# Optimization experiments

Hardware: AMD Instinct MI355X
Metric: run time of the kernel (lower is better)

Reference implementation:

```python
import jax, jax.numpy as jnp
import numpy as np

B, S, H, NH, DH, DFF = 4, 8192, 2048, 16, 128, 8192
K = 1024
EPS = 1e-5
THETA = 10000.0
SCALE_FACTOR = 1.0
SCALE_GAP = 1.0


def setup_inputs() -> dict:
    key = jax.random.key(0)
    ks = jax.random.split(key, 12)
    hidden_states = jax.random.normal(ks[0], (B, S, H), dtype=jnp.float32)
    position_ids = jnp.broadcast_to(jnp.arange(S, dtype=jnp.int32)[None, :], (B, S))
    # exactly K routed tokens per row -> static compacted length (matches torch
    # path when all rows have equal top-k counts)
    rowkeys = jax.random.split(ks[1], B)
    sel = jax.vmap(lambda k: jax.random.permutation(k, S)[:K])(rowkeys)  # [B,K]
    topk_mask = jnp.zeros((B, S), dtype=bool).at[jnp.arange(B)[:, None], sel].set(True)
    topk_scores = jax.random.uniform(ks[2], (B,), dtype=jnp.float32)
    w = lambda k, shp: (jax.random.normal(k, shp, dtype=jnp.float32) * 0.02)
    return {
        "hidden_states": hidden_states,
        "position_ids": position_ids,
        "topk_mask": topk_mask,
        "topk_scores": topk_scores,
        "topk_k": K,
        "Wq": w(ks[3], (H, H)),
        "Wk": w(ks[4], (H, H)),
        "Wv": w(ks[5], (H, H)),
        "Wo": w(ks[6], (H, H)),
        "Wgate": w(ks[7], (H, DFF)),
        "Wup": w(ks[8], (H, DFF)),
        "Wdown": w(ks[9], (DFF, H)),
        "ln1_w": jnp.ones((H,), dtype=jnp.float32),
        "ln2_w": jnp.ones((H,), dtype=jnp.float32),
    }


def _rmsnorm(x, w):
    return x * jax.lax.rsqrt(jnp.mean(x * x, axis=-1, keepdims=True) + EPS) * w


def _rotate_half(x):
    x1, x2 = jnp.split(x, 2, axis=-1)
    return jnp.concatenate([-x2, x1], axis=-1)


def reference(hidden_states, position_ids, topk_mask, topk_scores, topk_k,
              Wq, Wk, Wv, Wo, Wgate, Wup, Wdown, ln1_w, ln2_w):
    Kk = int(topk_k)
    b, s, h = hidden_states.shape
    # true positions first, in original order (stable) -> compacted indices
    order = jnp.argsort(jnp.where(topk_mask, 0, 1).astype(jnp.int32), axis=1, stable=True)
    topk_idx = order[:, :Kk]                              # [B,K]
    bidx = jnp.arange(b)[:, None]
    # 🔍 dispatch: gather routed tokens into compact [B,K,H]
    x = hidden_states[bidx, topk_idx]
    pos = position_ids[bidx, topk_idx]                    # original positions for RoPE

    residual = x
    hs = _rmsnorm(x, ln1_w)
    q = (hs @ Wq).reshape(b, Kk, NH, DH).transpose(0, 2, 1, 3)
    k = (hs @ Wk).reshape(b, Kk, NH, DH).transpose(0, 2, 1, 3)
    v = (hs @ Wv).reshape(b, Kk, NH, DH).transpose(0, 2, 1, 3)
    inv_freq = 1.0 / (THETA ** (jnp.arange(0, DH, 2, dtype=jnp.float32) / DH))
    freqs = pos[..., None].astype(jnp.float32) * inv_freq  # [B,K,DH/2]
    emb = jnp.concatenate([freqs, freqs], axis=-1)
    cos = jnp.cos(emb)[:, None, :, :]
    sin = jnp.sin(emb)[:, None, :, :]
    q = q * cos + _rotate_half(q) * sin
    k = k * cos + _rotate_half(k) * sin
    scores = jnp.einsum('bhqd,bhkd->bhqk', q, k) / np.sqrt(DH).astype(np.float32)
    causal = jnp.tril(jnp.ones((Kk, Kk), dtype=bool))
    scores = jnp.where(causal, scores, jnp.finfo(scores.dtype).min)
    attn = jax.nn.softmax(scores, axis=-1)
    o = jnp.einsum('bhqk,bhkd->bhqd', attn, v).transpose(0, 2, 1, 3).reshape(b, Kk, H)
    hs = residual + o @ Wo

    residual2 = hs
    m = _rmsnorm(hs, ln2_w)
    m = (jax.nn.silu(m @ Wgate) * (m @ Wup)) @ Wdown

    # rescale_hidden_states=True path
    scale = 0.5 * SCALE_FACTOR + (topk_scores - 0.5) * SCALE_GAP  # [B]
    out_gathered = residual2 + m * scale[:, None, None]
    # 🔍 combine: scatter routed outputs back; bottom tokens pass through unchanged
    out = hidden_states.at[bidx, topk_idx].set(out_gathered)
    return out
```

## Files before the change

### kernel.cpp

```cpp
#include <hip/hip_runtime.h>
#include <hip/hip_bf16.h>
#include <stdint.h>

#define Bb 4
#define Ss 8192
#define Hh 2048
#define NHh 16
#define DHh 128
#define DFFf 8192
#define KS 1024
#define NTOK 4096

typedef unsigned short u16;
typedef __bf16 bf16x8 __attribute__((ext_vector_type(8)));
typedef float f32x4 __attribute__((ext_vector_type(4)));

union B8 { uint4 u; bf16x8 v; u16 s[8]; };

__device__ __forceinline__ float b2f(u16 x) { return __uint_as_float(((unsigned)x) << 16); }
__device__ __forceinline__ u16 f2b(float x) {
  __hip_bfloat16 h = __float2bfloat16(x);
  return *reinterpret_cast<u16*>(&h);
}

__device__ __forceinline__ void gll16(const void* g, void* l) {
  __builtin_amdgcn_global_load_lds((const __attribute__((address_space(1))) void*)g,
                                   (__attribute__((address_space(3))) void*)l, 16, 0, 0);
}

__device__ __forceinline__ int swz16(int r, int cg) {
  int u = ((r & 1) << 2) | cg;
  return ((r >> 1) << 3) | (u ^ ((r >> 1) & 7));
}

__global__ void topk_prep(const void* maskp, const int* __restrict__ posids,
                          const float* __restrict__ scores,
                          int* __restrict__ idx, int* __restrict__ posg,
                          float* __restrict__ scalev) {
  int b = blockIdx.x;
  int tid = threadIdx.x, lane = tid & 63, wv = tid >> 6;
  __shared__ int wsum[4];
  __shared__ int base;
  __shared__ int mode;
  __shared__ int detCnt;
  if (tid == 0) { base = 0; detCnt = 0; }
  __syncthreads();
  {
    const unsigned char* mb = (const unsigned char*)maskp;
    int c = 0;
    for (int s = tid; s < 8192; s += 256) c += (mb[s] != 0);
    atomicAdd(&detCnt, c);
  }
  __syncthreads();
  if (tid == 0) mode = (detCnt == KS) ? 1 : 0;
  __syncthreads();
  const unsigned char* mb = (const unsigned char*)maskp;
  const int* mi = (const int*)maskp;
  for (int s0 = 0; s0 < Ss; s0 += 256) {
    int s = s0 + tid;
    int pred = mode ? (mb[(size_t)b * Ss + s] != 0) : (mi[(size_t)b * Ss + s] != 0);
    unsigned long long bal = __ballot(pred);
    int lp = __popcll(bal & ((1ull << lane) - 1ull));
    int wtot = __popcll(bal);
    if (lane == 0) wsum[wv] = wtot;
    __syncthreads();
    int woff = 0;
    for (int w = 0; w < wv; ++w) woff += wsum[w];
    int tot = wsum[0] + wsum[1] + wsum[2] + wsum[3];
    int p = base + woff + lp;
    if (pred && p < KS) {
      idx[b * KS + p] = s;
      posg[b * KS + p] = posids[(size_t)b * Ss + s];
    }
    __syncthreads();
    if (tid == 0) base += tot;
    __syncthreads();
  }
  if (b == 0 && tid < Bb) scalev[tid] = 0.5f * 1.0f + (scores[tid] - 0.5f) * 1.0f;
}

template <int MODE>
__global__ void transpose_w(const float* __restrict__ in, u16* __restrict__ out, int R, int C) {
  __shared__ float tile[32][33];
  int tx = threadIdx.x, ty = threadIdx.y;
  int c0 = blockIdx.x * 32, r0 = blockIdx.y * 32;
  for (int j = ty; j < 32; j += 8) tile[j][tx] = in[(size_t)(r0 + j) * C + c0 + tx];
  __syncthreads();
  for (int j = ty; j < 32; j += 8) {
    int c = c0 + j;
    size_t row = (MODE == 0) ? c : (size_t)((c >> 5) << 6) + (c & 31) + (MODE == 2 ? 32 : 0);
    out[row * R + r0 + tx] = f2b(tile[tx][j]);
  }
}

template <int GATHER>
__global__ __launch_bounds__(256) void rmsnorm_k(const float* __restrict__ src0,
                                                 const int* __restrict__ idx,
                                                 const float* __restrict__ w,
                                                 u16* __restrict__ out) {
  int t = blockIdx.x;
  const float* src;
  if (GATHER) { int b = t >> 10; src = src0 + ((size_t)b * Ss + idx[t]) * Hh; }
  else src = src0 + (size_t)t * Hh;
  int tid = threadIdx.x, lane = tid & 63, wv = tid >> 6;
  float4 x0 = *(const float4*)(src + tid * 8);
  float4 x1 = *(const float4*)(src + tid * 8 + 4);
  float ss = x0.x * x0.x + x0.y * x0.y + x0.z * x0.z + x0.w * x0.w +
             x1.x * x1.x + x1.y * x1.y + x1.z * x1.z + x1.w * x1.w;
  for (int o = 32; o; o >>= 1) ss += __shfl_down(ss, o);
  __shared__ float wred[4];
  if (lane == 0) wred[wv] = ss;
  __syncthreads();
  float tot = wred[0] + wred[1] + wred[2] + wred[3];
  float r = rsqrtf(tot * (1.0f / Hh) + 1e-5f);
  const float* wp = w + tid * 8;
  u16* op = out + (size_t)t * Hh + tid * 8;
  float xs[8] = {x0.x, x0.y, x0.z, x0.w, x1.x, x1.y, x1.z, x1.w};
#pragma unroll
  for (int j = 0; j < 8; ++j) op[j] = f2b(xs[j] * r * wp[j]);
}

template <int EPI>
__global__ __launch_bounds__(512, 2) void gemm256(
    const u16* __restrict__ A, const u16* __restrict__ Bt,
    int N, int Kd, int lda, int gm, int gw,
    u16* __restrict__ Cb,
    const float* __restrict__ hid, const int* __restrict__ idx,
    const float* __restrict__ hs2, const float* __restrict__ scalev,
    float* __restrict__ Cf) {
  __shared__ u16 lds[65536];
  int bid = blockIdx.x;
  int xcd = bid & 7;
  int i2 = bid >> 3;
  int bm = i2 / gw;
  int bn = xcd * gw + i2 % gw;
  int m0 = bm * 256, n0 = bn * 256;
  int tid = threadIdx.x, lane = tid & 63, wv = tid >> 6;
  int wm = wv >> 2, wn = wv & 3;
  int NT = Kd >> 6;

  int P16 = wv * 64 + lane;
  int blk = P16 >> 3, up = P16 & 7;
  int uu = up ^ (blk & 7);
  int r0 = blk * 2 + (uu >> 2), cg0 = uu & 3;
  const u16* srcA = A + (size_t)(m0 + r0) * lda + cg0 * 8;
  const u16* srcB = Bt + (size_t)(n0 + r0) * Kd + cg0 * 8;
  size_t rsA = (size_t)128 * lda, rsB = (size_t)128 * Kd;

  int offA = swz16(wm * 128 + (lane & 15), lane >> 4) * 8;
  int offB = 32768 + swz16(wn * 64 + (lane & 15), lane >> 4) * 8;
  u16* ldsw = &lds[wv * 512];

  f32x4 acc[8][4] = {};
  B8 aR[4], bR[4];

  gll16(srcB,      ldsw + 32768); gll16(srcB + rsB,      ldsw + 36864);
  gll16(srcA,      ldsw +     0); gll16(srcA + rsA,      ldsw +  4096);
  gll16(srcB + 32, ldsw + 40960); gll16(srcB + 32 + rsB, ldsw + 45056);
  gll16(srcA + 32, ldsw +  8192); gll16(srcA + 32 + rsA, ldsw + 12288);
  gll16(srcB + 64, ldsw + 49152); gll16(srcB + 64 + rsB, ldsw + 53248);
  gll16(srcA + 64, ldsw + 16384); gll16(srcA + 64 + rsA, ldsw + 20480);
  gll16(srcB + 96, ldsw + 57344); gll16(srcB + 96 + rsB, ldsw + 61440);
  asm volatile("s_waitcnt vmcnt(6)" ::: "memory");
  asm volatile("s_barrier" ::: "memory");

  const u16* stA = srcA + 64;
  const u16* stB = srcB + 64;

  auto phase = [&](int abase, int bbase, int mh) {
    if (mh == 0) {
#pragma unroll
      for (int nf = 0; nf < 4; ++nf) bR[nf].u = *(const uint4*)&lds[offB + bbase + nf * 512];
    }
#pragma unroll
    for (int i3 = 0; i3 < 4; ++i3)
      aR[i3].u = *(const uint4*)&lds[offA + abase + (i3 + 4 * mh) * 512];
  };
  auto mfma16 = [&](int mh) {
    asm volatile("s_barrier" ::: "memory");
    asm volatile("s_waitcnt lgkmcnt(0)" ::: "memory");
    __builtin_amdgcn_s_setprio(1);
#pragma unroll
    for (int nf = 0; nf < 4; ++nf)
#pragma unroll
      for (int i3 = 0; i3 < 4; ++i3)
        acc[mh * 4 + i3][nf] =
            __builtin_amdgcn_mfma_f32_16x16x32_bf16(aR[i3].v, bR[nf].v, acc[mh * 4 + i3][nf], 0, 0, 0);
    __builtin_amdgcn_s_setprio(0);
  };

  for (int ktp = 0; ktp < NT; ktp += 2) {
    bool sAll = (ktp < NT - 2);
    phase(0, 0, 0);
    { gll16(stA + 32, ldsw + 24576); gll16(stA + 32 + rsA, ldsw + 28672); }
    mfma16(0);
    asm volatile("s_barrier" ::: "memory");
    phase(0, 0, 1);
    if (sAll) { gll16(stB + 64, ldsw + 32768); gll16(stB + 64 + rsB, ldsw + 36864); }
    mfma16(1);
    asm volatile("s_barrier" ::: "memory");
    phase(8192, 8192, 0);
    if (sAll) { gll16(stA + 64, ldsw + 0); gll16(stA + 64 + rsA, ldsw + 4096); }
    mfma16(0);
    asm volatile("s_barrier" ::: "memory");
    phase(8192, 8192, 1);
    if (sAll) { gll16(stB + 96, ldsw + 40960); gll16(stB + 96 + rsB, ldsw + 45056); }
    mfma16(1);
    if (sAll) asm volatile("s_waitcnt vmcnt(6)" ::: "memory");
    else asm volatile("s_waitcnt vmcnt(0)" ::: "memory");
    asm volatile("s_barrier" ::: "memory");
    phase(16384, 16384, 0);
    if (sAll) { gll16(stA + 96, ldsw + 8192); gll16(stA + 96 + rsA, ldsw + 12288); }
    mfma16(0);
    asm volatile("s_barrier" ::: "memory");
    phase(16384, 16384, 1);
    if (sAll) { gll16(stB + 128, ldsw + 49152); gll16(stB + 128 + rsB, ldsw + 53248); }
    mfma16(1);
    asm volatile("s_barrier" ::: "memory");
    phase(24576, 24576, 0);
    if (sAll) { gll16(stA + 128, ldsw + 16384); gll16(stA + 128 + rsA, ldsw + 20480); }
    mfma16(0);
    asm volatile("s_barrier" ::: "memory");
    phase(24576, 24576, 1);
    if (sAll) { gll16(stB + 160, ldsw + 57344); gll16(stB + 160 + rsB, ldsw + 61440); }
    mfma16(1);
    if (sAll) asm volatile("s_waitcnt vmcnt(6)" ::: "memory");
    asm volatile("s_barrier" ::: "memory");
    stA += 128; stB += 128;
  }

  if (EPI == 4) {
    int gcol0 = ((n0 + wn * 64) >> 1) + (lane & 15);
#pragma unroll
    for (int mf = 0; mf < 8; ++mf) {
#pragma unroll
      for (int rr = 0; rr < 4; ++rr) {
        int row = m0 + wm * 128 + mf * 16 + (lane >> 4) * 4 + rr;
#pragma unroll
        for (int nf = 0; nf < 2; ++nf) {
          float g = acc[mf][nf][rr];
          float u = acc[mf][nf + 2][rr];
          Cb[(size_t)row * 8192 + gcol0 + nf * 16] = f2b(g / (1.0f + __expf(-g)) * u);
        }
      }
    }
    return;
  }

#pragma unroll
  for (int mf = 0; mf < 8; ++mf) {
#pragma unroll
    for (int rr = 0; rr < 4; ++rr) {
      int row = m0 + wm * 128 + mf * 16 + (lane >> 4) * 4 + rr;
#pragma unroll
      for (int nf = 0; nf < 4; ++nf) {
        int col = n0 + wn * 64 + nf * 16 + (lane & 15);
        float v = acc[mf][nf][rr];
        if (EPI == 0) {
          Cb[(size_t)row * N + col] = f2b(v);
        } else if (EPI == 1) {
          int b = row >> 10;
          Cf[(size_t)row * Hh + col] = hid[((size_t)b * Ss + idx[row]) * Hh + col] + v;
        } else {
          int b = row >> 10;
          Cf[((size_t)b * Ss + idx[row]) * Hh + col] = hs2[(size_t)row * Hh + col] + v * scalev[b];
        }
      }
    }
  }
}

template <int EPI>
__global__ __launch_bounds__(512, 2) void gemm128(
    const u16* __restrict__ A, const u16* __restrict__ Bt,
    int N, int Kd, int lda, int gm, int gw,
    u16* __restrict__ Cb,
    const float* __restrict__ hid, const int* __restrict__ idx,
    const float* __restrict__ hs2, const float* __restrict__ scalev,
    float* __restrict__ Cf, u16* __restrict__ vTout) {
  __shared__ u16 lds[49152];
  int bid = blockIdx.x;
  int xcd = bid & 7;
  int i2 = bid >> 3;
  int bm = i2 / gw;
  int bn = xcd * gw + i2 % gw;
  int m0 = bm * 128, n0 = bn * 256;
  int tid = threadIdx.x, lane = tid & 63, wv = tid >> 6;
  int wm = wv >> 2, wn = wv & 3;
  int NT = Kd >> 6;

  int P16 = wv * 64 + lane;
  int blk = P16 >> 3, up = P16 & 7;
  int uu = up ^ (blk & 7);
  int r0 = blk * 2 + (uu >> 2), cg0 = uu & 3;
  const u16* srcA = A + (size_t)(m0 + r0) * lda + cg0 * 8;
  const u16* srcB = Bt + (size_t)(n0 + r0) * Kd + cg0 * 8;
  size_t rsB = (size_t)128 * Kd;

  int offB = swz16(wn * 64 + (lane & 15), lane >> 4) * 8;
  int offA = 32768 + swz16(wm * 64 + (lane & 15), lane >> 4) * 8;
  u16* ldsw = &lds[wv * 512];

  f32x4 acc[4][4] = {};
  B8 aR[4], bR[4];

  gll16(srcB,      ldsw +     0); gll16(srcB + rsB,      ldsw +  4096); gll16(srcA,      ldsw + 32768);
  gll16(srcB + 32, ldsw +  8192); gll16(srcB + 32 + rsB, ldsw + 12288); gll16(srcA + 32, ldsw + 36864);
  gll16(srcB + 64, ldsw + 16384); gll16(srcB + 64 + rsB, ldsw + 20480); gll16(srcA + 64, ldsw + 40960);
  asm volatile("s_waitcnt vmcnt(6)" ::: "memory");
  asm volatile("s_barrier" ::: "memory");

  const u16* stA = srcA + 64;
  const u16* stB = srcB + 64;

  auto rd = [&](int s) {
#pragma unroll
    for (int f = 0; f < 4; ++f) bR[f].u = *(const uint4*)&lds[offB + s * 8192 + f * 512];
#pragma unroll
    for (int f = 0; f < 4; ++f) aR[f].u = *(const uint4*)&lds[offA + s * 4096 + f * 512];
  };
  auto mfma16 = [&]() {
    asm volatile("s_barrier" ::: "memory");
    asm volatile("s_waitcnt lgkmcnt(0)" ::: "memory");
    __builtin_amdgcn_s_setprio(1);
#pragma unroll
    for (int nf = 0; nf < 4; ++nf)
#pragma unroll
      for (int mf = 0; mf < 4; ++mf)
        acc[mf][nf] = __builtin_amdgcn_mfma_f32_16x16x32_bf16(aR[mf].v, bR[nf].v, acc[mf][nf], 0, 0, 0);
    __builtin_amdgcn_s_setprio(0);
  };

  for (int ktp = 0; ktp < NT; ktp += 2) {
    bool sAll = (ktp < NT - 2);
    rd(0);
    { gll16(stB + 32, ldsw + 24576); gll16(stB + 32 + rsB, ldsw + 28672); gll16(stA + 32, ldsw + 45056); }
    mfma16();
    asm volatile("s_waitcnt vmcnt(6)" ::: "memory");
    asm volatile("s_barrier" ::: "memory");
    rd(1);
    if (sAll) { gll16(stB + 64, ldsw + 0); gll16(stB + 64 + rsB, ldsw + 4096); gll16(stA + 64, ldsw + 32768); }
    mfma16();
    if (sAll) asm volatile("s_waitcnt vmcnt(6)" ::: "memory");
    else asm volatile("s_waitcnt vmcnt(3)" ::: "memory");
    asm volatile("s_barrier" ::: "memory");
    rd(2);
    if (sAll) { gll16(stB + 96, ldsw + 8192); gll16(stB + 96 + rsB, ldsw + 12288); gll16(stA + 96, ldsw + 36864); }
    mfma16();
    if (sAll) asm volatile("s_waitcnt vmcnt(6)" ::: "memory");
    else asm volatile("s_waitcnt vmcnt(0)" ::: "memory");
    asm volatile("s_barrier" ::: "memory");
    rd(3);
    if (sAll) { gll16(stB + 128, ldsw + 16384); gll16(stB + 128 + rsB, ldsw + 20480); gll16(stA + 128, ldsw + 40960); }
    mfma16();
    if (sAll) asm volatile("s_waitcnt vmcnt(6)" ::: "memory");
    asm volatile("s_barrier" ::: "memory");
    stA += 128; stB += 128;
  }

  if (EPI == 3) {
#pragma unroll
    for (int mf = 0; mf < 4; ++mf) {
      int rowb = m0 + wm * 64 + mf * 16 + (lane >> 4) * 4;
      int bb = rowb >> 10, kk2 = rowb & 1023;
#pragma unroll
      for (int nf = 0; nf < 4; ++nf) {
        int col = n0 + wn * 64 + nf * 16 + (lane & 15);
        if (col >= 4096) {
          int hh = (col - 4096) >> 7, dd = (col - 4096) & 127;
          ushort4 pk;
          pk.x = f2b(acc[mf][nf][0]); pk.y = f2b(acc[mf][nf][1]);
          pk.z = f2b(acc[mf][nf][2]); pk.w = f2b(acc[mf][nf][3]);
          *(ushort4*)&vTout[(((size_t)bb * 16 + hh) * 128 + dd) * 1024 + kk2] = pk;
        } else {
#pragma unroll
          for (int rr = 0; rr < 4; ++rr)
            Cb[(size_t)(rowb + rr) * N + col] = f2b(acc[mf][nf][rr]);
        }
      }
    }
    return;
  }

#pragma unroll
  for (int mf = 0; mf < 4; ++mf) {
#pragma unroll
    for (int rr = 0; rr < 4; ++rr) {
      int row = m0 + wm * 64 + mf * 16 + (lane >> 4) * 4 + rr;
#pragma unroll
      for (int nf = 0; nf < 4; ++nf) {
        int col = n0 + wn * 64 + nf * 16 + (lane & 15);
        float v = acc[mf][nf][rr];
        if (EPI == 0) {
          Cb[(size_t)row * N + col] = f2b(v);
        } else if (EPI == 1) {
          int b = row >> 10;
          Cf[(size_t)row * Hh + col] = hid[((size_t)b * Ss + idx[row]) * Hh + col] + v;
        } else {
          int b = row >> 10;
          Cf[((size_t)b * Ss + idx[row]) * Hh + col] = hs2[(size_t)row * Hh + col] + v * scalev[b];
        }
      }
    }
  }
}

__global__ __launch_bounds__(256) void rope_qk(u16* __restrict__ qkv,
                                               const int* __restrict__ posg) {
  int gid = blockIdx.x * 256 + threadIdx.x;
  int i = gid & 63;
  int h = (gid >> 6) & 15;
  int t = gid >> 10;
  float p = (float)posg[t];
  float inv = exp2f(-(float)i * (13.287712379549449f / 64.0f));
  float ang = p * inv;
  float sv, cv;
  __sincosf(ang, &sv, &cv);
  size_t base = (size_t)t * 6144 + h * DHh + i;
  u16* Q = qkv;
  u16* Kq = qkv + 2048;
  float q1 = b2f(Q[base]), q2 = b2f(Q[base + 64]);
  Q[base] = f2b(q1 * cv - q2 * sv);
  Q[base + 64] = f2b(q2 * cv + q1 * sv);
  float k1 = b2f(Kq[base]), k2 = b2f(Kq[base + 64]);
  Kq[base] = f2b(k1 * cv - k2 * sv);
  Kq[base + 64] = f2b(k2 * cv + k1 * sv);
}

__global__ __launch_bounds__(256) void attn_k(const u16* __restrict__ QKV,
                                              const u16* __restrict__ vT,
                                              u16* __restrict__ O) {
  int qb = blockIdx.x;
  int head = blockIdx.y;
  int b = head >> 4, h = head & 15;
  int tid = threadIdx.x, lane = tid & 63, wv = tid >> 6;
  int l15 = lane & 15, lq = lane >> 4, l7 = lane & 7;
  __shared__ __align__(16) u16 KsA[16384];
  __shared__ __align__(16) u16 VtA[16384];
  u16* PsB = &KsA[wv * 2176];

  int keyr = tid >> 4;
  int uphys = tid & 15;
  size_t koff0 = (size_t)keyr * 6144 + ((uphys ^ (keyr & 7)) * 8);
  size_t voff0 = (size_t)keyr * 1024 + ((uphys ^ (keyr & 7)) * 8);
  char* dK = (char*)KsA + wv * 1024;
  char* dV = (char*)VtA + wv * 1024;

  int q0 = qb * 64 + wv * 16;
  int tokQ = b * KS + q0;
  B8 qf[4];
  const u16* qp = QKV + (size_t)(tokQ + l15) * 6144 + h * DHh;
#pragma unroll
  for (int c = 0; c < 4; ++c) qf[c].u = *(const uint4*)(qp + c * 32 + lq * 8);
  float m_run = -1e30f, l_run = 0.0f;
  f32x4 oacc[8] = {};
  int qi = q0 + l15;

  int nt = (qb >> 1) + 1;
  for (int t = 0; t < nt; ++t) {
    int ks = t * 128;
    bool maskTile = (t == nt - 1);
    __syncthreads();
    const u16* kp = QKV + (size_t)(b * KS + ks) * 6144 + 2048 + h * DHh + koff0;
    const u16* vp = vT + ((size_t)head * 128) * 1024 + ks + voff0;
#pragma unroll
    for (int i = 0; i < 8; ++i) {
      gll16(kp + (size_t)i * 16 * 6144, dK + i * 4096);
      gll16(vp + (size_t)i * 16 * 1024, dV + i * 4096);
    }
    asm volatile("s_waitcnt vmcnt(0)" ::: "memory");
    __syncthreads();
    f32x4 st[8] = {};
#pragma unroll
    for (int c = 0; c < 4; ++c) {
#pragma unroll
      for (int kt = 0; kt < 8; ++kt) {
        B8 kf;
        kf.u = *(const uint4*)&KsA[(kt * 16 + l15) * 128 + (((c * 4 + lq) ^ l7) * 8)];
        st[kt] = __builtin_amdgcn_mfma_f32_16x16x32_bf16(kf.v, qf[c].v, st[kt], 0, 0, 0);
      }
    }
    __syncthreads();
    float pmax = -INFINITY;
    if (maskTile) {
#pragma unroll
      for (int kt = 0; kt < 8; ++kt)
#pragma unroll
        for (int r = 0; r < 4; ++r) {
          int ki = ks + kt * 16 + lq * 4 + r;
          float v = st[kt][r] * 0.088388347648318447f;
          v = (ki <= qi) ? v : -INFINITY;
          st[kt][r] = v;
          pmax = fmaxf(pmax, v);
        }
    } else {
#pragma unroll
      for (int kt = 0; kt < 8; ++kt)
#pragma unroll
        for (int r = 0; r < 4; ++r) {
          float v = st[kt][r] * 0.088388347648318447f;
          st[kt][r] = v;
          pmax = fmaxf(pmax, v);
        }
    }
    pmax = fmaxf(pmax, __shfl_xor(pmax, 16));
    pmax = fmaxf(pmax, __shfl_xor(pmax, 32));
    float m_new = fmaxf(m_run, pmax);
    float alpha = __expf(m_run - m_new);
    float psum = 0.0f;
#pragma unroll
    for (int kt = 0; kt < 8; ++kt)
#pragma unroll
      for (int r = 0; r < 4; ++r) {
        float pv = __expf(st[kt][r] - m_new);
        st[kt][r] = pv;
        psum += pv;
      }
    psum += __shfl_xor(psum, 16);
    psum += __shfl_xor(psum, 32);
    l_run = l_run * alpha + psum;
    m_run = m_new;
#pragma unroll
    for (int kt = 0; kt < 8; ++kt) {
      ushort4 pk;
      pk.x = f2b(st[kt][0]); pk.y = f2b(st[kt][1]);
      pk.z = f2b(st[kt][2]); pk.w = f2b(st[kt][3]);
      *(ushort4*)&PsB[l15 * 136 + kt * 16 + lq * 4] = pk;
    }
    B8 pf[4];
#pragma unroll
    for (int kslot = 0; kslot < 4; ++kslot)
      pf[kslot].u = *(const uint4*)&PsB[l15 * 136 + kslot * 32 + lq * 8];
    float al0 = __shfl(alpha, lq * 4 + 0);
    float al1 = __shfl(alpha, lq * 4 + 1);
    float al2 = __shfl(alpha, lq * 4 + 2);
    float al3 = __shfl(alpha, lq * 4 + 3);
#pragma unroll
    for (int dt = 0; dt < 8; ++dt) {
      oacc[dt][0] *= al0; oacc[dt][1] *= al1;
      oacc[dt][2] *= al2; oacc[dt][3] *= al3;
    }
#pragma unroll
    for (int dt = 0; dt < 8; ++dt) {
      int d = dt * 16 + l15;
#pragma unroll
      for (int kslot = 0; kslot < 4; ++kslot) {
        B8 vf;
        vf.u = *(const uint4*)&VtA[d * 128 + (((kslot * 4 + lq) ^ l7) * 8)];
        oacc[dt] = __builtin_amdgcn_mfma_f32_16x16x32_bf16(pf[kslot].v, vf.v, oacc[dt], 0, 0, 0);
      }
    }
  }
  float linv = 1.0f / l_run;
  float li[4];
#pragma unroll
  for (int r = 0; r < 4; ++r) li[r] = __shfl(linv, lq * 4 + r);
#pragma unroll
  for (int r = 0; r < 4; ++r) {
    int tok = tokQ + lq * 4 + r;
    u16* op = O + (size_t)tok * Hh + h * DHh;
#pragma unroll
    for (int dt = 0; dt < 8; ++dt) op[dt * 16 + l15] = f2b(oacc[dt][r] * li[r]);
  }
}

extern "C" void kernel_launch(void* const* d_in, const int* in_sizes, int n_in,
                              void* d_out, int out_size, void* d_ws, size_t ws_size,
                              hipStream_t stream) {
  (void)in_sizes; (void)n_in; (void)out_size; (void)ws_size;
  const float* hid = (const float*)d_in[0];
  const int* posids = (const int*)d_in[1];
  const void* mask = d_in[2];
  const float* scores = (const float*)d_in[3];
  const float* Wq = (const float*)d_in[5];
  const float* Wk = (const float*)d_in[6];
  const float* Wv = (const float*)d_in[7];
  const float* Wo = (const float*)d_in[8];
  const float* Wg = (const float*)d_in[9];
  const float* Wu = (const float*)d_in[10];
  const float* Wd = (const float*)d_in[11];
  const float* ln1 = (const float*)d_in[12];
  const float* ln2 = (const float*)d_in[13];
  float* out = (float*)d_out;
  char* ws = (char*)d_ws;

  u16* WqkvT = (u16*)(ws + 0);
  u16* WoT   = (u16*)(ws + 25165824);
  u16* WguT  = (u16*)(ws + 33554432);
  u16* WdT   = (u16*)(ws + 100663296);
  int* idx   = (int*)(ws + 134217728);
  int* posg  = (int*)(ws + 134217728 + 16384);
  float* scalev = (float*)(ws + 134217728 + 32768);
  char* R = ws + 134283264;
  u16* hsn    = (u16*)(R);
  u16* qkv    = (u16*)(R + 16777216);
  u16* attn_o = (u16*)(R + 67108864);
  u16* vT     = (u16*)(R + 88080384);
  u16* gu2    = (u16*)(R);
  float* hs2  = (float*)(ws + 268500992);
  u16* mnorm  = (u16*)(ws + 302055424);

  hipMemcpyAsync(out, hid, (size_t)Bb * Ss * Hh * 4, hipMemcpyDeviceToDevice, stream);

  topk_prep<<<Bb, 256, 0, stream>>>(mask, posids, scores, idx, posg, scalev);

  transpose_w<0><<<dim3(64, 64), dim3(32, 8), 0, stream>>>(Wq, WqkvT, 2048, 2048);
  transpose_w<0><<<dim3(64, 64), dim3(32, 8), 0, stream>>>(Wk, WqkvT + 2048 * 2048, 2048, 2048);
  transpose_w<0><<<dim3(64, 64), dim3(32, 8), 0, stream>>>(Wv, WqkvT + 4096 * 2048, 2048, 2048);
  transpose_w<0><<<dim3(64, 64), dim3(32, 8), 0, stream>>>(Wo, WoT, 2048, 2048);
  transpose_w<1><<<dim3(256, 64), dim3(32, 8), 0, stream>>>(Wg, WguT, 2048, 8192);
  transpose_w<2><<<dim3(256, 64), dim3(32, 8), 0, stream>>>(Wu, WguT, 2048, 8192);
  transpose_w<0><<<dim3(64, 256), dim3(32, 8), 0, stream>>>(Wd, WdT, 8192, 2048);

  rmsnorm_k<1><<<NTOK, 256, 0, stream>>>(hid, idx, ln1, hsn);

  gemm128<3><<<768, 512, 0, stream>>>(hsn, WqkvT, 6144, 2048, 2048, 32, 3, qkv,
                                      nullptr, nullptr, nullptr, nullptr, nullptr, vT);

  rope_qk<<<16384, 256, 0, stream>>>(qkv, posg);

  attn_k<<<dim3(16, 64), 256, 0, stream>>>(qkv, vT, attn_o);

  gemm128<1><<<256, 512, 0, stream>>>(attn_o, WoT, 2048, 2048, 2048, 32, 1, nullptr,
                                      hid, idx, nullptr, nullptr, hs2, nullptr);

  rmsnorm_k<0><<<NTOK, 256, 0, stream>>>(hs2, nullptr, ln2, mnorm);

  gemm256<4><<<1024, 512, 0, stream>>>(mnorm, WguT, 16384, 2048, 2048, 16, 8, gu2,
                                       nullptr, nullptr, nullptr, nullptr, nullptr);

  gemm128<2><<<256, 512, 0, stream>>>(gu2, WdT, 2048, 8192, 8192, 32, 1, nullptr,
                                      nullptr, idx, hs2, scalev, out, nullptr);
}
```

Before: 1.076 ms.

## Retune gemm128 pipeline, keep P in registers in attention, split gate/up GEMM

```diff
diff --git a/kernel.cpp b/kernel.cpp
--- a/kernel.cpp
+++ b/kernel.cpp
@@ -123,7 +123,7 @@
 template <int EPI>
 __global__ __launch_bounds__(512, 2) void gemm256(
     const u16* __restrict__ A, const u16* __restrict__ Bt,
-    int N, int Kd, int lda, int gm, int gw,
+    int N, int Kd, int lda, int gm, int gw, int nb,
     u16* __restrict__ Cb,
     const float* __restrict__ hid, const int* __restrict__ idx,
     const float* __restrict__ hs2, const float* __restrict__ scalev,
@@ -133,7 +133,7 @@
   int xcd = bid & 7;
   int i2 = bid >> 3;
   int bm = i2 / gw;
-  int bn = xcd * gw + i2 % gw;
+  int bn = xcd * gw + i2 % gw + nb;
   int m0 = bm * 256, n0 = bn * 256;
   int tid = threadIdx.x, lane = tid & 63, wv = tid >> 6;
   int wm = wv >> 2, wn = wv & 3;
@@ -271,14 +271,14 @@
 }
 
 template <int EPI>
-__global__ __launch_bounds__(512, 2) void gemm128(
+__global__ __launch_bounds__(512, 4) void gemm128(
     const u16* __restrict__ A, const u16* __restrict__ Bt,
     int N, int Kd, int lda, int gm, int gw,
     u16* __restrict__ Cb,
     const float* __restrict__ hid, const int* __restrict__ idx,
     const float* __restrict__ hs2, const float* __restrict__ scalev,
     float* __restrict__ Cf, u16* __restrict__ vTout) {
-  __shared__ u16 lds[49152];
+  __shared__ u16 lds[36864];
   int bid = blockIdx.x;
   int xcd = bid & 7;
   int i2 = bid >> 3;
@@ -288,6 +288,7 @@
   int tid = threadIdx.x, lane = tid & 63, wv = tid >> 6;
   int wm = wv >> 2, wn = wv & 3;
   int NT = Kd >> 6;
+  int P = NT * 2;
 
   int P16 = wv * 64 + lane;
   int blk = P16 >> 3, up = P16 & 7;
@@ -298,28 +299,32 @@
   size_t rsB = (size_t)128 * Kd;
 
   int offB = swz16(wn * 64 + (lane & 15), lane >> 4) * 8;
-  int offA = 32768 + swz16(wm * 64 + (lane & 15), lane >> 4) * 8;
+  int offA = swz16(wm * 64 + (lane & 15), lane >> 4) * 8;
   u16* ldsw = &lds[wv * 512];
 
   f32x4 acc[4][4] = {};
   B8 aR[4], bR[4];
 
-  gll16(srcB,      ldsw +     0); gll16(srcB + rsB,      ldsw +  4096); gll16(srcA,      ldsw + 32768);
-  gll16(srcB + 32, ldsw +  8192); gll16(srcB + 32 + rsB, ldsw + 12288); gll16(srcA + 32, ldsw + 36864);
-  gll16(srcB + 64, ldsw + 16384); gll16(srcB + 64 + rsB, ldsw + 20480); gll16(srcA + 64, ldsw + 40960);
-  asm volatile("s_waitcnt vmcnt(6)" ::: "memory");
+  auto stage = [&](int q, int bB, int aB) {
+    const u16* spB = srcB + q * 32;
+    gll16(spB, ldsw + bB);
+    gll16(spB + rsB, ldsw + bB + 4096);
+    gll16(srcA + q * 32, ldsw + aB);
+  };
+
+  stage(0, 0, 24576);
+  stage(1, 8192, 28672);
+  asm volatile("s_waitcnt vmcnt(3)" ::: "memory");
   asm volatile("s_barrier" ::: "memory");
 
-  const u16* stA = srcA + 64;
-  const u16* stB = srcB + 64;
-
-  auto rd = [&](int s) {
-#pragma unroll
-    for (int f = 0; f < 4; ++f) bR[f].u = *(const uint4*)&lds[offB + s * 8192 + f * 512];
-#pragma unroll
-    for (int f = 0; f < 4; ++f) aR[f].u = *(const uint4*)&lds[offA + s * 4096 + f * 512];
-  };
-  auto mfma16 = [&]() {
+  int rB = 0, rA = 24576;
+  int tB = 16384, tA = 32768;
+  for (int p = 0; p < P; ++p) {
+#pragma unroll
+    for (int f = 0; f < 4; ++f) bR[f].u = *(const uint4*)&lds[rB + offB + f * 512];
+#pragma unroll
+    for (int f = 0; f < 4; ++f) aR[f].u = *(const uint4*)&lds[rA + offA + f * 512];
+    if (p + 2 < P) stage(p + 2, tB, tA);
     asm volatile("s_barrier" ::: "memory");
     asm volatile("s_waitcnt lgkmcnt(0)" ::: "memory");
     __builtin_amdgcn_s_setprio(1);
@@ -329,33 +334,12 @@
       for (int mf = 0; mf < 4; ++mf)
         acc[mf][nf] = __builtin_amdgcn_mfma_f32_16x16x32_bf16(aR[mf].v, bR[nf].v, acc[mf][nf], 0, 0, 0);
     __builtin_amdgcn_s_setprio(0);
-  };
-
-  for (int ktp = 0; ktp < NT; ktp += 2) {
-    bool sAll = (ktp < NT - 2);
-    rd(0);
-    { gll16(stB + 32, ldsw + 24576); gll16(stB + 32 + rsB, ldsw + 28672); gll16(stA + 32, ldsw + 45056); }
-    mfma16();
-    asm volatile("s_waitcnt vmcnt(6)" ::: "memory");
-    asm volatile("s_barrier" ::: "memory");
-    rd(1);
-    if (sAll) { gll16(stB + 64, ldsw + 0); gll16(stB + 64 + rsB, ldsw + 4096); gll16(stA + 64, ldsw + 32768); }
-    mfma16();
-    if (sAll) asm volatile("s_waitcnt vmcnt(6)" ::: "memory");
-    else asm volatile("s_waitcnt vmcnt(3)" ::: "memory");
-    asm volatile("s_barrier" ::: "memory");
-    rd(2);
-    if (sAll) { gll16(stB + 96, ldsw + 8192); gll16(stB + 96 + rsB, ldsw + 12288); gll16(stA + 96, ldsw + 36864); }
-    mfma16();
-    if (sAll) asm volatile("s_waitcnt vmcnt(6)" ::: "memory");
-    else asm volatile("s_waitcnt vmcnt(0)" ::: "memory");
-    asm volatile("s_barrier" ::: "memory");
-    rd(3);
-    if (sAll) { gll16(stB + 128, ldsw + 16384); gll16(stB + 128 + rsB, ldsw + 20480); gll16(stA + 128, ldsw + 40960); }
-    mfma16();
-    if (sAll) asm volatile("s_waitcnt vmcnt(6)" ::: "memory");
-    asm volatile("s_barrier" ::: "memory");
-    stA += 128; stB += 128;
+    if (p < P - 2) asm volatile("s_waitcnt vmcnt(3)" ::: "memory");
+    else if (p == P - 2) asm volatile("s_waitcnt vmcnt(0)" ::: "memory");
+    asm volatile("s_barrier" ::: "memory");
+    tB = rB; tA = rA;
+    rB = (rB == 16384) ? 0 : rB + 8192;
+    rA = (rA == 32768) ? 24576 : rA + 4096;
   }
 
   if (EPI == 3) {
@@ -363,6 +347,8 @@
     for (int mf = 0; mf < 4; ++mf) {
       int rowb = m0 + wm * 64 + mf * 16 + (lane >> 4) * 4;
       int bb = rowb >> 10, kk2 = rowb & 1023;
+      int w = kk2 & 127;
+      int kk2p = (kk2 & ~127) | (((((w >> 5) & 3) << 2) + ((w >> 2) & 3)) << 3) | (((w >> 4) & 1) << 2);
 #pragma unroll
       for (int nf = 0; nf < 4; ++nf) {
         int col = n0 + wn * 64 + nf * 16 + (lane & 15);
@@ -371,7 +357,7 @@
           ushort4 pk;
           pk.x = f2b(acc[mf][nf][0]); pk.y = f2b(acc[mf][nf][1]);
           pk.z = f2b(acc[mf][nf][2]); pk.w = f2b(acc[mf][nf][3]);
-          *(ushort4*)&vTout[(((size_t)bb * 16 + hh) * 128 + dd) * 1024 + kk2] = pk;
+          *(ushort4*)&vTout[(((size_t)bb * 16 + hh) * 128 + dd) * 1024 + kk2p] = pk;
         } else {
 #pragma unroll
           for (int rr = 0; rr < 4; ++rr)
@@ -437,12 +423,11 @@
   int l15 = lane & 15, lq = lane >> 4, l7 = lane & 7;
   __shared__ __align__(16) u16 KsA[16384];
   __shared__ __align__(16) u16 VtA[16384];
-  u16* PsB = &KsA[wv * 2176];
-
-  int keyr = tid >> 4;
-  int uphys = tid & 15;
-  size_t koff0 = (size_t)keyr * 6144 + ((uphys ^ (keyr & 7)) * 8);
-  size_t voff0 = (size_t)keyr * 1024 + ((uphys ^ (keyr & 7)) * 8);
+
+  int rr0 = tid >> 4;
+  int u0 = tid & 15;
+  size_t koff0 = (size_t)rr0 * 6144 + ((u0 ^ (rr0 & 7)) * 8);
+  size_t voff0 = (size_t)rr0 * 1024 + ((u0 ^ (rr0 & 7)) * 8);
   char* dK = (char*)KsA + wv * 1024;
   char* dV = (char*)VtA + wv * 1024;
 
@@ -462,13 +447,12 @@
     bool maskTile = (t == nt - 1);
     __syncthreads();
     const u16* kp = QKV + (size_t)(b * KS + ks) * 6144 + 2048 + h * DHh + koff0;
-    const u16* vp = vT + ((size_t)head * 128) * 1024 + ks + voff0;
-#pragma unroll
-    for (int i = 0; i < 8; ++i) {
-      gll16(kp + (size_t)i * 16 * 6144, dK + i * 4096);
-      gll16(vp + (size_t)i * 16 * 1024, dV + i * 4096);
-    }
-    asm volatile("s_waitcnt vmcnt(0)" ::: "memory");
+    const u16* vp = vT + (size_t)head * 131072 + ks + voff0;
+#pragma unroll
+    for (int i = 0; i < 8; ++i) gll16(kp + (size_t)i * 98304, dK + i * 4096);
+#pragma unroll
+    for (int i = 0; i < 8; ++i) gll16(vp + i * 16384, dV + i * 4096);
+    asm volatile("s_waitcnt vmcnt(8)" ::: "memory");
     __syncthreads();
     f32x4 st[8] = {};
 #pragma unroll
@@ -480,7 +464,6 @@
         st[kt] = __builtin_amdgcn_mfma_f32_16x16x32_bf16(kf.v, qf[c].v, st[kt], 0, 0, 0);
       }
     }
-    __syncthreads();
     float pmax = -INFINITY;
     if (maskTile) {
 #pragma unroll
@@ -520,17 +503,16 @@
     psum += __shfl_xor(psum, 32);
     l_run = l_run * alpha + psum;
     m_run = m_new;
-#pragma unroll
-    for (int kt = 0; kt < 8; ++kt) {
-      ushort4 pk;
-      pk.x = f2b(st[kt][0]); pk.y = f2b(st[kt][1]);
-      pk.z = f2b(st[kt][2]); pk.w = f2b(st[kt][3]);
-      *(ushort4*)&PsB[l15 * 136 + kt * 16 + lq * 4] = pk;
-    }
+    asm volatile("s_waitcnt vmcnt(0)" ::: "memory");
+    __syncthreads();
     B8 pf[4];
 #pragma unroll
     for (int kslot = 0; kslot < 4; ++kslot)
-      pf[kslot].u = *(const uint4*)&PsB[l15 * 136 + kslot * 32 + lq * 8];
+#pragma unroll
+      for (int j = 0; j < 4; ++j) {
+        pf[kslot].s[j] = f2b(st[2 * kslot][j]);
+        pf[kslot].s[4 + j] = f2b(st[2 * kslot + 1][j]);
+      }
     float al0 = __shfl(alpha, lq * 4 + 0);
     float al1 = __shfl(alpha, lq * 4 + 1);
     float al2 = __shfl(alpha, lq * 4 + 2);
@@ -626,8 +608,10 @@
 
   rmsnorm_k<0><<<NTOK, 256, 0, stream>>>(hs2, nullptr, ln2, mnorm);
 
-  gemm256<4><<<1024, 512, 0, stream>>>(mnorm, WguT, 16384, 2048, 2048, 16, 8, gu2,
-                                       nullptr, nullptr, nullptr, nullptr, nullptr);
+  gemm256<4><<<512, 512, 0, stream>>>(mnorm, WguT, 16384, 2048, 2048, 16, 4, 0, gu2,
+                                      nullptr, nullptr, nullptr, nullptr, nullptr);
+  gemm256<4><<<512, 512, 0, stream>>>(mnorm, WguT, 16384, 2048, 2048, 16, 4, 32, gu2,
+                                      nullptr, nullptr, nullptr, nullptr, nullptr);
 
   gemm128<2><<<256, 512, 0, stream>>>(gu2, WdT, 2048, 8192, 8192, 32, 1, nullptr,
                                       nullptr, idx, hs2, scalev, out, nullptr);
```

Result: faster. 1.035 ms (-3.8%).
